# Kernel optimization log

Hardware: AMD Instinct MI355X
Metric: run time of the kernel (lower is better)

## Reference

```python
import jax, jax.numpy as jnp
import numpy as np

H = 16
E = 2048
LAT = E // 4
D = E // H          # 128
R = D // 2          # 64 (rotary dim)
B, S = 2, 2048

def _lin(x, W, b):
    return x @ W.T + b

def _rope_cos_sin(seq_len):
    inv_freq = 1.0 / (10000.0 ** (jnp.arange(0, R, 2, dtype=jnp.float32) / R))  # (R/2,)
    t = jnp.arange(seq_len, dtype=jnp.float32)
    freqs = jnp.outer(t, inv_freq)                 # (S, R/2)
    emb = jnp.concatenate([freqs, freqs], axis=-1) # (S, R)
    return jnp.cos(emb), jnp.sin(emb)

def _rotate_half(x):
    x1, x2 = x[..., : R // 2], x[..., R // 2 :]
    return jnp.concatenate([-x2, x1], axis=-1)

def _apply_rope(x, cos, sin):
    # x: (B, S, H, R); cos/sin: (S, R)
    c = cos[None, :, None, :]
    s = sin[None, :, None, :]
    return x * c + _rotate_half(x) * s

def setup_inputs() -> dict:
    key = jax.random.key(0)
    ks = jax.random.split(key, 20)
    def w(k, o, i):
        return jax.random.normal(k, (o, i), dtype=jnp.float32) * 0.02
    def bvec(k, o):
        return jax.random.normal(k, (o,), dtype=jnp.float32) * 0.02
    return {
        "x": jax.random.normal(ks[0], (B, S, E), dtype=jnp.float32),
        "Wkv_d": w(ks[1], LAT, E), "bkv_d": bvec(ks[2], LAT),
        "Wq_d": w(ks[3], LAT, E), "bq_d": bvec(ks[4], LAT),
        "Wk_u": w(ks[5], E // 2, LAT), "bk_u": bvec(ks[6], E // 2),
        "Wq_u": w(ks[7], E // 2, LAT), "bq_u": bvec(ks[8], E // 2),
        "Wv_u": w(ks[9], E, LAT), "bv_u": bvec(ks[10], E),
        "Wrk": w(ks[11], E // 2, E), "brk": bvec(ks[12], E // 2),
        "Wrq": w(ks[13], E // 2, LAT), "brq": bvec(ks[14], E // 2),
        "Wo": w(ks[15], E, E), "bo": bvec(ks[16], E),
    }

def reference(x, Wkv_d, bkv_d, Wq_d, bq_d, Wk_u, bk_u, Wq_u, bq_u,
              Wv_u, bv_u, Wrk, brk, Wrq, brq, Wo, bo):
    Bn, Sn, _ = x.shape
    kv_d = _lin(x, Wkv_d, bkv_d)                      # (B,S,LAT)
    q_d = _lin(x, Wq_d, bq_d)                         # (B,S,LAT)
    k1 = _lin(kv_d, Wk_u, bk_u).reshape(Bn, Sn, H, R)
    q1 = _lin(q_d, Wq_u, bq_u).reshape(Bn, Sn, H, R)
    v = _lin(kv_d, Wv_u, bv_u).reshape(Bn, Sn, H, D)
    kr = _lin(x, Wrk, brk).reshape(Bn, Sn, H, R)
    qr = _lin(q_d, Wrq, brq).reshape(Bn, Sn, H, R)
    cos, sin = _rope_cos_sin(Sn)
    qr = _apply_rope(qr, cos, sin)
    kr = _apply_rope(kr, cos, sin)
    k = jnp.concatenate([k1, kr], axis=-1)            # (B,S,H,D)
    q = jnp.concatenate([q1, qr], axis=-1)
    scale = 1.0 / np.sqrt(D)
    attn = jnp.einsum("bqhd,bkhd->bhqk", q, k) * scale
    attn = jax.nn.softmax(attn, axis=-1)
    out = jnp.einsum("bhqk,bkhd->bqhd", attn, v).reshape(Bn, Sn, E)
    return _lin(out, Wo, bo)
```

## Files before the change

kernel.cpp:

```cpp
#include <hip/hip_runtime.h>
#include <cmath>

typedef unsigned short ushort_t;
typedef unsigned int u32;
typedef __attribute__((ext_vector_type(8))) __bf16 bf16x8;
typedef __attribute__((ext_vector_type(4))) float f32x4;

#define Hh 16
#define Ss 2048
#define SCALE 0.08838834764831845f

__device__ __forceinline__ ushort_t f2bf(float f) {
  union { float f; unsigned u; } c; c.f = f;
  unsigned u = c.u;
  return (ushort_t)((u + 0x7FFFu + ((u >> 16) & 1u)) >> 16);
}
__device__ __forceinline__ float bf2f(ushort_t h) {
  union { unsigned u; float f; } c; c.u = ((unsigned)h) << 16;
  return c.f;
}
__device__ __forceinline__ u32 cvt_pk_bf16(float lo, float hi) {
  u32 r;
  asm volatile("v_cvt_pk_bf16_f32 %0, %1, %2" : "=v"(r) : "v"(lo), "v"(hi));
  return r;
}

__device__ __forceinline__ void gload_lds16(const ushort_t* g, ushort_t* l) {
  __builtin_amdgcn_global_load_lds(
      (const __attribute__((address_space(1))) u32*)g,
      (__attribute__((address_space(3))) u32*)l, 16, 0, 0);
}

struct SrcPtrs { const float* p[9]; };

__global__ __launch_bounds__(256) void convert_all_kernel(SrcPtrs sp,
    ushort_t* __restrict__ x_bf, ushort_t* __restrict__ wbuf) {
  const int cum[9] = {8192, 9216, 10240, 12288, 12800, 13824, 14336, 14848, 18944};
  const int dsto[9] = {0, 0, 1048576, 2097152, 4194304, 4718592, 5767168, 6291456, 6815744};
  const int bid = blockIdx.x;
  int s = 0;
  #pragma unroll
  for (int i = 0; i < 8; ++i) s += (bid >= cum[i]);
  const int lb = bid - (s == 0 ? 0 : cum[s - 1]);
  const float* src = sp.p[s] + (size_t)lb * 1024;
  ushort_t* dst = (s == 0 ? x_bf : wbuf + dsto[s]) + (size_t)lb * 1024;
  const int i = threadIdx.x * 4;
  float4 v = *(const float4*)&src[i];
  ushort4 o;
  o.x = f2bf(v.x); o.y = f2bf(v.y); o.z = f2bf(v.z); o.w = f2bf(v.w);
  *(ushort4*)&dst[i] = o;
}

template<int MODE, typename OUTT>
__global__ __launch_bounds__(256) void gemm_bf16(
    const ushort_t* __restrict__ A, const ushort_t* __restrict__ W,
    const float* __restrict__ bias, OUTT* __restrict__ C0,
    ushort_t* __restrict__ C1, int K)
{
  __shared__ ushort_t As[128][32];
  __shared__ ushort_t Bs[128][32];
  const int tid = threadIdx.x;
  const int lane = tid & 63;
  const int w = tid >> 6;
  const int wr = w >> 1, wc = w & 1;
  const int l15 = lane & 15, lhi = lane >> 4;
  const int m0 = blockIdx.y * 128, n0 = blockIdx.x * 128;

  const int srow = w * 16 + (lane >> 2);
  const int schunk = (lane & 3) * 8;

  f32x4 acc[4][4];
  #pragma unroll
  for (int i = 0; i < 4; ++i)
    #pragma unroll
    for (int j = 0; j < 4; ++j)
      acc[i][j] = (f32x4){0.f, 0.f, 0.f, 0.f};

  for (int k0 = 0; k0 < K; k0 += 32) {
    __syncthreads();
    gload_lds16(&A[(size_t)(m0 + srow) * K + k0 + schunk],       &As[w * 16][0]);
    gload_lds16(&A[(size_t)(m0 + 64 + srow) * K + k0 + schunk],  &As[64 + w * 16][0]);
    gload_lds16(&W[(size_t)(n0 + srow) * K + k0 + schunk],       &Bs[w * 16][0]);
    gload_lds16(&W[(size_t)(n0 + 64 + srow) * K + k0 + schunk],  &Bs[64 + w * 16][0]);
    __syncthreads();
    bf16x8 af[4], bfr[4];
    #pragma unroll
    for (int i = 0; i < 4; ++i) af[i] = *(const bf16x8*)&As[wr * 64 + i * 16 + l15][lhi * 8];
    #pragma unroll
    for (int j = 0; j < 4; ++j) bfr[j] = *(const bf16x8*)&Bs[wc * 64 + j * 16 + l15][lhi * 8];
    #pragma unroll
    for (int i = 0; i < 4; ++i)
      #pragma unroll
      for (int j = 0; j < 4; ++j)
        acc[i][j] = __builtin_amdgcn_mfma_f32_16x16x32_bf16(af[i], bfr[j], acc[i][j], 0, 0, 0);
  }

  #pragma unroll
  for (int i = 0; i < 4; ++i) {
    #pragma unroll
    for (int j = 0; j < 4; ++j) {
      const int n = n0 + wc * 64 + j * 16 + l15;
      const float bz = bias[n];
      #pragma unroll
      for (int r = 0; r < 4; ++r) {
        const int m = m0 + wr * 64 + i * 16 + lhi * 4 + r;
        const float v = acc[i][j][r] + bz;
        if constexpr (MODE == 0) {
          C0[(size_t)m * 2048 + n] = v;
        } else if constexpr (MODE == 2) {
          if (n < 1024)
            C0[(size_t)(n >> 9) * 2097152 + (size_t)m * 512 + (n & 511)] = (OUTT)f2bf(v);
          else {
            const int np = n - 1024;
            C1[(size_t)m * 2048 + (np >> 6) * 128 + (np & 63)] = f2bf(v);
          }
        } else if constexpr (MODE == 3) {
          if (n < 1024)
            C0[(size_t)m * 2048 + (n >> 6) * 128 + (n & 63)] = (OUTT)f2bf(v);
          else {
            const int np = n - 1024;
            C1[(size_t)(m >> 11) * 4194304 + (size_t)np * 2048 + (m & 2047)] = f2bf(v);
          }
        } else {
          const int np = n & 1023;
          C0[(size_t)m * 2048 + (np >> 6) * 128 + (np & 63) + ((n >> 10) << 6)] = (OUTT)f2bf(v);
        }
      }
    }
  }
}

__global__ __launch_bounds__(256) void rope_bf16_kernel(ushort_t* __restrict__ q,
                                                        ushort_t* __restrict__ k) {
  const int t = threadIdx.x & 63;
  const int idx = blockIdx.x * 4 + (threadIdx.x >> 6);
  const int s = (idx >> 4) & (Ss - 1);
  ushort_t* base = (t < 32 ? q : k) + (size_t)idx * 128 + 64;
  const int i = t & 31;
  const float invf = expf(-logf(10000.f) * (float)i / 32.f);
  const float fr = (float)s * invf;
  const float cs = cosf(fr), sn = sinf(fr);
  const float x1 = bf2f(base[i]);
  const float x2 = bf2f(base[i + 32]);
  base[i]      = f2bf(x1 * cs - x2 * sn);
  base[i + 32] = f2bf(x2 * cs + x1 * sn);
}

__global__ __launch_bounds__(256) void flash_mfma_kernel(
    const ushort_t* __restrict__ Qb, const ushort_t* __restrict__ Kb,
    const ushort_t* __restrict__ Vt, ushort_t* __restrict__ Oattn)
{
  __shared__ ushort_t Ks[64][136];
  __shared__ ushort_t Vs[128][72];
  __shared__ ushort_t Ps[4][32][72];

  const int tid = threadIdx.x, lane = tid & 63, w = tid >> 6;
  const int l15 = lane & 15, lhi = lane >> 4;
  const int bh = blockIdx.y, b = bh >> 4, h = bh & 15;
  const int q0 = blockIdx.x * 128 + w * 32;

  bf16x8 qf[2][4];
  #pragma unroll
  for (int mi = 0; mi < 2; ++mi) {
    const size_t qrow = (size_t)b * Ss + q0 + mi * 16 + l15;
    const ushort_t* qp = Qb + (qrow * Hh + h) * 128;
    #pragma unroll
    for (int dk = 0; dk < 4; ++dk)
      qf[mi][dk] = *(const bf16x8*)(qp + dk * 32 + lhi * 8);
  }

  f32x4 o[2][8];
  #pragma unroll
  for (int mi = 0; mi < 2; ++mi)
    #pragma unroll
    for (int dn = 0; dn < 8; ++dn) o[mi][dn] = (f32x4){0.f, 0.f, 0.f, 0.f};
  float lsum[2] = {0.f, 0.f};

  const size_t kbase_g = (size_t)b * Ss * 2048 + (size_t)h * 128;
  const size_t vbase_g = (size_t)bh * 128 * Ss;

  bf16x8 kv[4], vv[4];
  #pragma unroll
  for (int p = 0; p < 4; ++p) {
    const int idx = p * 256 + tid;
    kv[p] = *(const bf16x8*)&Kb[kbase_g + (size_t)(idx >> 4) * 2048 + (idx & 15) * 8];
    vv[p] = *(const bf16x8*)&Vt[vbase_g + (size_t)(idx >> 3) * Ss + (idx & 7) * 8];
  }

  for (int t = 0; t < Ss / 64; ++t) {
    __syncthreads();
    #pragma unroll
    for (int p = 0; p < 4; ++p) {
      const int idx = p * 256 + tid;
      *(bf16x8*)&Ks[idx >> 4][(idx & 15) * 8] = kv[p];
      *(bf16x8*)&Vs[idx >> 3][(idx & 7) * 8] = vv[p];
    }
    __syncthreads();

    if (t + 1 < Ss / 64) {
      const int s1 = (t + 1) * 64;
      #pragma unroll
      for (int p = 0; p < 4; ++p) {
        const int idx = p * 256 + tid;
        kv[p] = *(const bf16x8*)&Kb[kbase_g + (size_t)(s1 + (idx >> 4)) * 2048 + (idx & 15) * 8];
        vv[p] = *(const bf16x8*)&Vt[vbase_g + (size_t)(idx >> 3) * Ss + s1 + (idx & 7) * 8];
      }
    }

    f32x4 s[2][4];
    #pragma unroll
    for (int mi = 0; mi < 2; ++mi)
      #pragma unroll
      for (int jc = 0; jc < 4; ++jc) s[mi][jc] = (f32x4){0.f, 0.f, 0.f, 0.f};
    #pragma unroll
    for (int jc = 0; jc < 4; ++jc)
      #pragma unroll
      for (int dk = 0; dk < 4; ++dk) {
        bf16x8 ak = *(const bf16x8*)&Ks[jc * 16 + l15][dk * 32 + lhi * 8];
        s[0][jc] = __builtin_amdgcn_mfma_f32_16x16x32_bf16(ak, qf[0][dk], s[0][jc], 0, 0, 0);
        s[1][jc] = __builtin_amdgcn_mfma_f32_16x16x32_bf16(ak, qf[1][dk], s[1][jc], 0, 0, 0);
      }

    #pragma unroll
    for (int mi = 0; mi < 2; ++mi)
      #pragma unroll
      for (int jc = 0; jc < 4; ++jc) {
        const float p0 = __expf(s[mi][jc][0] * SCALE);
        const float p1 = __expf(s[mi][jc][1] * SCALE);
        const float p2 = __expf(s[mi][jc][2] * SCALE);
        const float p3 = __expf(s[mi][jc][3] * SCALE);
        lsum[mi] += (p0 + p1) + (p2 + p3);
        const u32 d0 = cvt_pk_bf16(p0, p1);
        const u32 d1 = cvt_pk_bf16(p2, p3);
        *(uint2*)&Ps[w][mi * 16 + l15][jc * 16 + lhi * 4] = make_uint2(d0, d1);
      }

    #pragma unroll
    for (int kc = 0; kc < 2; ++kc) {
      bf16x8 ap0 = *(const bf16x8*)&Ps[w][l15][kc * 32 + lhi * 8];
      bf16x8 ap1 = *(const bf16x8*)&Ps[w][16 + l15][kc * 32 + lhi * 8];
      #pragma unroll
      for (int dn = 0; dn < 8; ++dn) {
        bf16x8 bv = *(const bf16x8*)&Vs[dn * 16 + l15][kc * 32 + lhi * 8];
        o[0][dn] = __builtin_amdgcn_mfma_f32_16x16x32_bf16(ap0, bv, o[0][dn], 0, 0, 0);
        o[1][dn] = __builtin_amdgcn_mfma_f32_16x16x32_bf16(ap1, bv, o[1][dn], 0, 0, 0);
      }
    }
  }

  #pragma unroll
  for (int mi = 0; mi < 2; ++mi) {
    float v = lsum[mi];
    v += __shfl_xor(v, 16);
    v += __shfl_xor(v, 32);
    lsum[mi] = v;
  }

  #pragma unroll
  for (int mi = 0; mi < 2; ++mi) {
    float inv[4];
    #pragma unroll
    for (int r = 0; r < 4; ++r)
      inv[r] = 1.f / __shfl(lsum[mi], lhi * 4 + r);
    #pragma unroll
    for (int dn = 0; dn < 8; ++dn)
      #pragma unroll
      for (int r = 0; r < 4; ++r) {
        const int row = q0 + mi * 16 + lhi * 4 + r;
        const size_t addr = ((size_t)b * Ss + row) * 2048 + h * 128 + dn * 16 + l15;
        Oattn[addr] = f2bf(o[mi][dn][r] * inv[r]);
      }
  }
}

extern "C" void kernel_launch(void* const* d_in, const int* in_sizes, int n_in,
                              void* d_out, int out_size, void* d_ws, size_t ws_size,
                              hipStream_t stream)
{
  const float* x     = (const float*)d_in[0];
  const float* Wkv_d = (const float*)d_in[1];
  const float* bkv_d = (const float*)d_in[2];
  const float* Wq_d  = (const float*)d_in[3];
  const float* bq_d  = (const float*)d_in[4];
  const float* Wk_u  = (const float*)d_in[5];
  const float* bk_u  = (const float*)d_in[6];
  const float* Wq_u  = (const float*)d_in[7];
  const float* bq_u  = (const float*)d_in[8];
  const float* Wv_u  = (const float*)d_in[9];
  const float* bv_u  = (const float*)d_in[10];
  const float* Wrk   = (const float*)d_in[11];
  const float* brk   = (const float*)d_in[12];
  const float* Wrq   = (const float*)d_in[13];
  const float* brq   = (const float*)d_in[14];
  const float* Wo    = (const float*)d_in[15];
  const float* bo    = (const float*)d_in[16];

  ushort_t* ws = (ushort_t*)d_ws;
  ushort_t* x_bf  = ws;
  ushort_t* kv_d  = ws + 8388608;
  ushort_t* q_d   = ws + 10485760;
  ushort_t* qb    = ws + 12582912;
  ushort_t* kb    = ws + 20971520;
  ushort_t* vt    = ws + 29360128;
  ushort_t* attn  = ws + 37748736;
  ushort_t* wbuf  = ws + 46137344;
  float* bias_x  = (float*)(ws + 57147392);
  float* bias_kv = (float*)(ws + 57151488);
  float* bias_q  = (float*)(ws + 57157632);

  SrcPtrs sp;
  sp.p[0] = x;    sp.p[1] = Wkv_d; sp.p[2] = Wq_d; sp.p[3] = Wrk;
  sp.p[4] = Wk_u; sp.p[5] = Wv_u;  sp.p[6] = Wq_u; sp.p[7] = Wrq;
  sp.p[8] = Wo;
  convert_all_kernel<<<dim3(18944), dim3(256), 0, stream>>>(sp, x_bf, wbuf);

  hipMemcpyAsync(bias_x,         bkv_d, 512 * 4,  hipMemcpyDeviceToDevice, stream);
  hipMemcpyAsync(bias_x + 512,   bq_d,  512 * 4,  hipMemcpyDeviceToDevice, stream);
  hipMemcpyAsync(bias_x + 1024,  brk,   1024 * 4, hipMemcpyDeviceToDevice, stream);
  hipMemcpyAsync(bias_kv,        bk_u,  1024 * 4, hipMemcpyDeviceToDevice, stream);
  hipMemcpyAsync(bias_kv + 1024, bv_u,  2048 * 4, hipMemcpyDeviceToDevice, stream);
  hipMemcpyAsync(bias_q,         bq_u,  1024 * 4, hipMemcpyDeviceToDevice, stream);
  hipMemcpyAsync(bias_q + 1024,  brq,   1024 * 4, hipMemcpyDeviceToDevice, stream);

  const dim3 blk(256);

  gemm_bf16<2, ushort_t><<<dim3(16, 32), blk, 0, stream>>>(
      x_bf, wbuf, bias_x, kv_d, kb + 64, 2048);
  gemm_bf16<3, ushort_t><<<dim3(24, 32), blk, 0, stream>>>(
      kv_d, wbuf + 4194304, bias_kv, kb, vt, 512);
  gemm_bf16<4, ushort_t><<<dim3(16, 32), blk, 0, stream>>>(
      q_d, wbuf + 5767168, bias_q, qb, nullptr, 512);

  rope_bf16_kernel<<<dim3(Ss * Hh * 2 / 4), blk, 0, stream>>>(qb, kb);

  flash_mfma_kernel<<<dim3(Ss / 128, 32), blk, 0, stream>>>(qb, kb, vt, attn);

  gemm_bf16<0, float><<<dim3(16, 32), blk, 0, stream>>>(
      attn, wbuf + 6815744, bo, (float*)d_out, nullptr, 2048);
}
```

Measured before the change: 292.1 us.

## Double-buffer flash K/V tiles, keep P in registers, merge up-projection GEMMs

The flash attention kernel now double-buffers its K/V tiles in LDS, which needs one barrier per iteration instead of two. It rebuilds the probability MFMA operand in registers with permlane swaps instead of bouncing it through a per-wave LDS buffer. The K/V and Q up-projection GEMMs are merged into one launch that switches its A pointer by column block. This removes a kernel launch and some LDS traffic, at the cost of more LDS per block and correctness that depends on the permlane layout and the block-dependent A offset.

```diff
diff --git a/kernel.cpp b/kernel.cpp
--- a/kernel.cpp
+++ b/kernel.cpp
@@ -55,7 +55,7 @@
 __global__ __launch_bounds__(256) void gemm_bf16(
     const ushort_t* __restrict__ A, const ushort_t* __restrict__ W,
     const float* __restrict__ bias, OUTT* __restrict__ C0,
-    ushort_t* __restrict__ C1, int K)
+    ushort_t* __restrict__ C1, ushort_t* __restrict__ C2, int K)
 {
   __shared__ ushort_t As[128][32];
   __shared__ ushort_t Bs[128][32];
@@ -65,6 +65,8 @@
   const int wr = w >> 1, wc = w & 1;
   const int l15 = lane & 15, lhi = lane >> 4;
   const int m0 = blockIdx.y * 128, n0 = blockIdx.x * 128;
+
+  if constexpr (MODE == 5) { if (blockIdx.x >= 24) A += 2097152; }
 
   const int srow = w * 16 + (lane >> 2);
   const int schunk = (lane & 3) * 8;
@@ -114,16 +116,17 @@
             const int np = n - 1024;
             C1[(size_t)m * 2048 + (np >> 6) * 128 + (np & 63)] = f2bf(v);
           }
-        } else if constexpr (MODE == 3) {
-          if (n < 1024)
+        } else {
+          if (n < 1024) {
             C0[(size_t)m * 2048 + (n >> 6) * 128 + (n & 63)] = (OUTT)f2bf(v);
-          else {
+          } else if (n < 3072) {
             const int np = n - 1024;
             C1[(size_t)(m >> 11) * 4194304 + (size_t)np * 2048 + (m & 2047)] = f2bf(v);
+          } else {
+            const int np = n - 3072;
+            const int col = ((np & 1023) >> 6) * 128 + (np & 63) + ((np >> 10) << 6);
+            C2[(size_t)m * 2048 + col] = f2bf(v);
           }
-        } else {
-          const int np = n & 1023;
-          C0[(size_t)m * 2048 + (np >> 6) * 128 + (np & 63) + ((n >> 10) << 6)] = (OUTT)f2bf(v);
         }
       }
     }
@@ -150,9 +153,8 @@
     const ushort_t* __restrict__ Qb, const ushort_t* __restrict__ Kb,
     const ushort_t* __restrict__ Vt, ushort_t* __restrict__ Oattn)
 {
-  __shared__ ushort_t Ks[64][136];
-  __shared__ ushort_t Vs[128][72];
-  __shared__ ushort_t Ps[4][32][72];
+  __shared__ ushort_t Ks[2][64][136];
+  __shared__ ushort_t Vs[2][128][72];
 
   const int tid = threadIdx.x, lane = tid & 63, w = tid >> 6;
   const int l15 = lane & 15, lhi = lane >> 4;
@@ -180,32 +182,32 @@
   const size_t vbase_g = (size_t)bh * 128 * Ss;
 
   bf16x8 kv[4], vv[4];
-  #pragma unroll
-  for (int p = 0; p < 4; ++p) {
-    const int idx = p * 256 + tid;
-    kv[p] = *(const bf16x8*)&Kb[kbase_g + (size_t)(idx >> 4) * 2048 + (idx & 15) * 8];
-    vv[p] = *(const bf16x8*)&Vt[vbase_g + (size_t)(idx >> 3) * Ss + (idx & 7) * 8];
-  }
-
-  for (int t = 0; t < Ss / 64; ++t) {
-    __syncthreads();
+  auto load_tile = [&](int s0) {
     #pragma unroll
     for (int p = 0; p < 4; ++p) {
       const int idx = p * 256 + tid;
-      *(bf16x8*)&Ks[idx >> 4][(idx & 15) * 8] = kv[p];
-      *(bf16x8*)&Vs[idx >> 3][(idx & 7) * 8] = vv[p];
+      kv[p] = *(const bf16x8*)&Kb[kbase_g + (size_t)(s0 + (idx >> 4)) * 2048 + (idx & 15) * 8];
+      vv[p] = *(const bf16x8*)&Vt[vbase_g + (size_t)(idx >> 3) * Ss + s0 + (idx & 7) * 8];
     }
-    __syncthreads();
-
-    if (t + 1 < Ss / 64) {
-      const int s1 = (t + 1) * 64;
-      #pragma unroll
-      for (int p = 0; p < 4; ++p) {
-        const int idx = p * 256 + tid;
-        kv[p] = *(const bf16x8*)&Kb[kbase_g + (size_t)(s1 + (idx >> 4)) * 2048 + (idx & 15) * 8];
-        vv[p] = *(const bf16x8*)&Vt[vbase_g + (size_t)(idx >> 3) * Ss + s1 + (idx & 7) * 8];
-      }
+  };
+  auto write_tile = [&](int buf) {
+    #pragma unroll
+    for (int p = 0; p < 4; ++p) {
+      const int idx = p * 256 + tid;
+      *(bf16x8*)&Ks[buf][idx >> 4][(idx & 15) * 8] = kv[p];
+      *(bf16x8*)&Vs[buf][idx >> 3][(idx & 7) * 8] = vv[p];
     }
+  };
+
+  load_tile(0);
+  write_tile(0);
+  load_tile(64);
+  __syncthreads();
+
+  for (int t = 0; t < Ss / 64; ++t) {
+    const int cur = t & 1, nxt = cur ^ 1;
+    write_tile(nxt);
+    load_tile(t + 2 < Ss / 64 ? (t + 2) * 64 : Ss - 64);
 
     f32x4 s[2][4];
     #pragma unroll
@@ -216,13 +218,14 @@
     for (int jc = 0; jc < 4; ++jc)
       #pragma unroll
       for (int dk = 0; dk < 4; ++dk) {
-        bf16x8 ak = *(const bf16x8*)&Ks[jc * 16 + l15][dk * 32 + lhi * 8];
+        bf16x8 ak = *(const bf16x8*)&Ks[cur][jc * 16 + l15][dk * 32 + lhi * 8];
         s[0][jc] = __builtin_amdgcn_mfma_f32_16x16x32_bf16(ak, qf[0][dk], s[0][jc], 0, 0, 0);
         s[1][jc] = __builtin_amdgcn_mfma_f32_16x16x32_bf16(ak, qf[1][dk], s[1][jc], 0, 0, 0);
       }
 
     #pragma unroll
-    for (int mi = 0; mi < 2; ++mi)
+    for (int mi = 0; mi < 2; ++mi) {
+      u32 D0[4], D1[4];
       #pragma unroll
       for (int jc = 0; jc < 4; ++jc) {
         const float p0 = __expf(s[mi][jc][0] * SCALE);
@@ -230,22 +233,27 @@
         const float p2 = __expf(s[mi][jc][2] * SCALE);
         const float p3 = __expf(s[mi][jc][3] * SCALE);
         lsum[mi] += (p0 + p1) + (p2 + p3);
-        const u32 d0 = cvt_pk_bf16(p0, p1);
-        const u32 d1 = cvt_pk_bf16(p2, p3);
-        *(uint2*)&Ps[w][mi * 16 + l15][jc * 16 + lhi * 4] = make_uint2(d0, d1);
-      }
-
-    #pragma unroll
-    for (int kc = 0; kc < 2; ++kc) {
-      bf16x8 ap0 = *(const bf16x8*)&Ps[w][l15][kc * 32 + lhi * 8];
-      bf16x8 ap1 = *(const bf16x8*)&Ps[w][16 + l15][kc * 32 + lhi * 8];
-      #pragma unroll
-      for (int dn = 0; dn < 8; ++dn) {
-        bf16x8 bv = *(const bf16x8*)&Vs[dn * 16 + l15][kc * 32 + lhi * 8];
-        o[0][dn] = __builtin_amdgcn_mfma_f32_16x16x32_bf16(ap0, bv, o[0][dn], 0, 0, 0);
-        o[1][dn] = __builtin_amdgcn_mfma_f32_16x16x32_bf16(ap1, bv, o[1][dn], 0, 0, 0);
+        D0[jc] = cvt_pk_bf16(p0, p1);
+        D1[jc] = cvt_pk_bf16(p2, p3);
+      }
+      #pragma unroll
+      for (int kc = 0; kc < 2; ++kc) {
+        u32 X = D0[2 * kc], Xp = D0[2 * kc + 1];
+        u32 Y = D1[2 * kc], Yp = D1[2 * kc + 1];
+        asm volatile("v_permlane32_swap_b32 %0, %1" : "+v"(X), "+v"(Xp));
+        asm volatile("v_permlane16_swap_b32 %0, %1" : "+v"(X), "+v"(Xp));
+        asm volatile("v_permlane32_swap_b32 %0, %1" : "+v"(Y), "+v"(Yp));
+        asm volatile("v_permlane16_swap_b32 %0, %1" : "+v"(Y), "+v"(Yp));
+        union { u32 u[4]; bf16x8 v; } ap;
+        ap.u[0] = X; ap.u[1] = Y; ap.u[2] = Xp; ap.u[3] = Yp;
+        #pragma unroll
+        for (int dn = 0; dn < 8; ++dn) {
+          bf16x8 bv = *(const bf16x8*)&Vs[cur][dn * 16 + l15][kc * 32 + lhi * 8];
+          o[mi][dn] = __builtin_amdgcn_mfma_f32_16x16x32_bf16(ap.v, bv, o[mi][dn], 0, 0, 0);
+        }
       }
     }
+    __syncthreads();
   }
 
   #pragma unroll
@@ -304,9 +312,8 @@
   ushort_t* vt    = ws + 29360128;
   ushort_t* attn  = ws + 37748736;
   ushort_t* wbuf  = ws + 46137344;
-  float* bias_x  = (float*)(ws + 57147392);
-  float* bias_kv = (float*)(ws + 57151488);
-  float* bias_q  = (float*)(ws + 57157632);
+  float* bias_x   = (float*)(ws + 57147392);
+  float* bias_kvq = (float*)(ws + 57151488);
 
   SrcPtrs sp;
   sp.p[0] = x;    sp.p[1] = Wkv_d; sp.p[2] = Wq_d; sp.p[3] = Wrk;
@@ -314,27 +321,25 @@
   sp.p[8] = Wo;
   convert_all_kernel<<<dim3(18944), dim3(256), 0, stream>>>(sp, x_bf, wbuf);
 
-  hipMemcpyAsync(bias_x,         bkv_d, 512 * 4,  hipMemcpyDeviceToDevice, stream);
-  hipMemcpyAsync(bias_x + 512,   bq_d,  512 * 4,  hipMemcpyDeviceToDevice, stream);
-  hipMemcpyAsync(bias_x + 1024,  brk,   1024 * 4, hipMemcpyDeviceToDevice, stream);
-  hipMemcpyAsync(bias_kv,        bk_u,  1024 * 4, hipMemcpyDeviceToDevice, stream);
-  hipMemcpyAsync(bias_kv + 1024, bv_u,  2048 * 4, hipMemcpyDeviceToDevice, stream);
-  hipMemcpyAsync(bias_q,         bq_u,  1024 * 4, hipMemcpyDeviceToDevice, stream);
-  hipMemcpyAsync(bias_q + 1024,  brq,   1024 * 4, hipMemcpyDeviceToDevice, stream);
+  hipMemcpyAsync(bias_x,          bkv_d, 512 * 4,  hipMemcpyDeviceToDevice, stream);
+  hipMemcpyAsync(bias_x + 512,    bq_d,  512 * 4,  hipMemcpyDeviceToDevice, stream);
+  hipMemcpyAsync(bias_x + 1024,   brk,   1024 * 4, hipMemcpyDeviceToDevice, stream);
+  hipMemcpyAsync(bias_kvq,        bk_u,  1024 * 4, hipMemcpyDeviceToDevice, stream);
+  hipMemcpyAsync(bias_kvq + 1024, bv_u,  2048 * 4, hipMemcpyDeviceToDevice, stream);
+  hipMemcpyAsync(bias_kvq + 3072, bq_u,  1024 * 4, hipMemcpyDeviceToDevice, stream);
+  hipMemcpyAsync(bias_kvq + 4096, brq,   1024 * 4, hipMemcpyDeviceToDevice, stream);
 
   const dim3 blk(256);
 
   gemm_bf16<2, ushort_t><<<dim3(16, 32), blk, 0, stream>>>(
-      x_bf, wbuf, bias_x, kv_d, kb + 64, 2048);
-  gemm_bf16<3, ushort_t><<<dim3(24, 32), blk, 0, stream>>>(
-      kv_d, wbuf + 4194304, bias_kv, kb, vt, 512);
-  gemm_bf16<4, ushort_t><<<dim3(16, 32), blk, 0, stream>>>(
-      q_d, wbuf + 5767168, bias_q, qb, nullptr, 512);
+      x_bf, wbuf, bias_x, kv_d, kb + 64, nullptr, 2048);
+  gemm_bf16<5, ushort_t><<<dim3(40, 32), blk, 0, stream>>>(
+      kv_d, wbuf + 4194304, bias_kvq, kb, vt, qb, 512);
 
   rope_bf16_kernel<<<dim3(Ss * Hh * 2 / 4), blk, 0, stream>>>(qb, kb);
 
   flash_mfma_kernel<<<dim3(Ss / 128, 32), blk, 0, stream>>>(qb, kb, vt, attn);
 
   gemm_bf16<0, float><<<dim3(16, 32), blk, 0, stream>>>(
-      attn, wbuf + 6815744, bo, (float*)d_out, nullptr, 2048);
-}
+      attn, wbuf + 6815744, bo, (float*)d_out, nullptr, nullptr, 2048);
+}
```

Measured after the change: 327.9 us. 1.12x slower.

## Merge kv/q up-projection GEMMs into one launch and deepen K tile to 64

Applied to the files above, without the earlier changes.

Combines the two up-projection GEMMs (kv_d→k/v and q_d→q) into a single launch with 40 column blocks. Blocks past column 24 offset the A pointer to q_d and write into qb through a new third output pointer. The GEMM K-step also doubles from 32 to 64 with wider LDS tiles, which halves the number of barrier pairs per tile. The aim is less launch overhead, a better-filled grid and lower sync cost, at the price of twice the LDS per block, which could reduce occupancy.

```diff
diff --git a/kernel.cpp b/kernel.cpp
--- a/kernel.cpp
+++ b/kernel.cpp
@@ -55,10 +55,10 @@
 __global__ __launch_bounds__(256) void gemm_bf16(
     const ushort_t* __restrict__ A, const ushort_t* __restrict__ W,
     const float* __restrict__ bias, OUTT* __restrict__ C0,
-    ushort_t* __restrict__ C1, int K)
+    ushort_t* __restrict__ C1, ushort_t* __restrict__ C2, int K)
 {
-  __shared__ ushort_t As[128][32];
-  __shared__ ushort_t Bs[128][32];
+  __shared__ ushort_t As[128][64];
+  __shared__ ushort_t Bs[128][64];
   const int tid = threadIdx.x;
   const int lane = tid & 63;
   const int w = tid >> 6;
@@ -66,8 +66,10 @@
   const int l15 = lane & 15, lhi = lane >> 4;
   const int m0 = blockIdx.y * 128, n0 = blockIdx.x * 128;
 
-  const int srow = w * 16 + (lane >> 2);
-  const int schunk = (lane & 3) * 8;
+  if constexpr (MODE == 5) { if (blockIdx.x >= 24) A += 2097152; }
+
+  const int srow_base = w * 8 + (lane >> 3);
+  const int scol = (lane & 7) * 8;
 
   f32x4 acc[4][4];
   #pragma unroll
@@ -76,23 +78,30 @@
     for (int j = 0; j < 4; ++j)
       acc[i][j] = (f32x4){0.f, 0.f, 0.f, 0.f};
 
-  for (int k0 = 0; k0 < K; k0 += 32) {
+  for (int k0 = 0; k0 < K; k0 += 64) {
     __syncthreads();
-    gload_lds16(&A[(size_t)(m0 + srow) * K + k0 + schunk],       &As[w * 16][0]);
-    gload_lds16(&A[(size_t)(m0 + 64 + srow) * K + k0 + schunk],  &As[64 + w * 16][0]);
-    gload_lds16(&W[(size_t)(n0 + srow) * K + k0 + schunk],       &Bs[w * 16][0]);
-    gload_lds16(&W[(size_t)(n0 + 64 + srow) * K + k0 + schunk],  &Bs[64 + w * 16][0]);
+    #pragma unroll
+    for (int q = 0; q < 4; ++q) {
+      const int row = q * 32 + srow_base;
+      gload_lds16(&A[(size_t)(m0 + row) * K + k0 + scol], &As[q * 32 + w * 8][0]);
+      gload_lds16(&W[(size_t)(n0 + row) * K + k0 + scol], &Bs[q * 32 + w * 8][0]);
+    }
     __syncthreads();
-    bf16x8 af[4], bfr[4];
-    #pragma unroll
-    for (int i = 0; i < 4; ++i) af[i] = *(const bf16x8*)&As[wr * 64 + i * 16 + l15][lhi * 8];
-    #pragma unroll
-    for (int j = 0; j < 4; ++j) bfr[j] = *(const bf16x8*)&Bs[wc * 64 + j * 16 + l15][lhi * 8];
-    #pragma unroll
-    for (int i = 0; i < 4; ++i)
+    #pragma unroll
+    for (int dk = 0; dk < 2; ++dk) {
+      bf16x8 af[4], bfr[4];
+      #pragma unroll
+      for (int i = 0; i < 4; ++i)
+        af[i] = *(const bf16x8*)&As[wr * 64 + i * 16 + l15][dk * 32 + lhi * 8];
       #pragma unroll
       for (int j = 0; j < 4; ++j)
-        acc[i][j] = __builtin_amdgcn_mfma_f32_16x16x32_bf16(af[i], bfr[j], acc[i][j], 0, 0, 0);
+        bfr[j] = *(const bf16x8*)&Bs[wc * 64 + j * 16 + l15][dk * 32 + lhi * 8];
+      #pragma unroll
+      for (int i = 0; i < 4; ++i)
+        #pragma unroll
+        for (int j = 0; j < 4; ++j)
+          acc[i][j] = __builtin_amdgcn_mfma_f32_16x16x32_bf16(af[i], bfr[j], acc[i][j], 0, 0, 0);
+    }
   }
 
   #pragma unroll
@@ -114,16 +123,17 @@
             const int np = n - 1024;
             C1[(size_t)m * 2048 + (np >> 6) * 128 + (np & 63)] = f2bf(v);
           }
-        } else if constexpr (MODE == 3) {
-          if (n < 1024)
+        } else {
+          if (n < 1024) {
             C0[(size_t)m * 2048 + (n >> 6) * 128 + (n & 63)] = (OUTT)f2bf(v);
-          else {
+          } else if (n < 3072) {
             const int np = n - 1024;
             C1[(size_t)(m >> 11) * 4194304 + (size_t)np * 2048 + (m & 2047)] = f2bf(v);
+          } else {
+            const int np = n - 3072;
+            const int col = ((np & 1023) >> 6) * 128 + (np & 63) + ((np >> 10) << 6);
+            C2[(size_t)m * 2048 + col] = f2bf(v);
           }
-        } else {
-          const int np = n & 1023;
-          C0[(size_t)m * 2048 + (np >> 6) * 128 + (np & 63) + ((n >> 10) << 6)] = (OUTT)f2bf(v);
         }
       }
     }
@@ -304,9 +314,8 @@
   ushort_t* vt    = ws + 29360128;
   ushort_t* attn  = ws + 37748736;
   ushort_t* wbuf  = ws + 46137344;
-  float* bias_x  = (float*)(ws + 57147392);
-  float* bias_kv = (float*)(ws + 57151488);
-  float* bias_q  = (float*)(ws + 57157632);
+  float* bias_x   = (float*)(ws + 57147392);
+  float* bias_kvq = (float*)(ws + 57151488);
 
   SrcPtrs sp;
   sp.p[0] = x;    sp.p[1] = Wkv_d; sp.p[2] = Wq_d; sp.p[3] = Wrk;
@@ -314,27 +323,25 @@
   sp.p[8] = Wo;
   convert_all_kernel<<<dim3(18944), dim3(256), 0, stream>>>(sp, x_bf, wbuf);
 
-  hipMemcpyAsync(bias_x,         bkv_d, 512 * 4,  hipMemcpyDeviceToDevice, stream);
-  hipMemcpyAsync(bias_x + 512,   bq_d,  512 * 4,  hipMemcpyDeviceToDevice, stream);
-  hipMemcpyAsync(bias_x + 1024,  brk,   1024 * 4, hipMemcpyDeviceToDevice, stream);
-  hipMemcpyAsync(bias_kv,        bk_u,  1024 * 4, hipMemcpyDeviceToDevice, stream);
-  hipMemcpyAsync(bias_kv + 1024, bv_u,  2048 * 4, hipMemcpyDeviceToDevice, stream);
-  hipMemcpyAsync(bias_q,         bq_u,  1024 * 4, hipMemcpyDeviceToDevice, stream);
-  hipMemcpyAsync(bias_q + 1024,  brq,   1024 * 4, hipMemcpyDeviceToDevice, stream);
+  hipMemcpyAsync(bias_x,          bkv_d, 512 * 4,  hipMemcpyDeviceToDevice, stream);
+  hipMemcpyAsync(bias_x + 512,    bq_d,  512 * 4,  hipMemcpyDeviceToDevice, stream);
+  hipMemcpyAsync(bias_x + 1024,   brk,   1024 * 4, hipMemcpyDeviceToDevice, stream);
+  hipMemcpyAsync(bias_kvq,        bk_u,  1024 * 4, hipMemcpyDeviceToDevice, stream);
+  hipMemcpyAsync(bias_kvq + 1024, bv_u,  2048 * 4, hipMemcpyDeviceToDevice, stream);
+  hipMemcpyAsync(bias_kvq + 3072, bq_u,  1024 * 4, hipMemcpyDeviceToDevice, stream);
+  hipMemcpyAsync(bias_kvq + 4096, brq,   1024 * 4, hipMemcpyDeviceToDevice, stream);
 
   const dim3 blk(256);
 
   gemm_bf16<2, ushort_t><<<dim3(16, 32), blk, 0, stream>>>(
-      x_bf, wbuf, bias_x, kv_d, kb + 64, 2048);
-  gemm_bf16<3, ushort_t><<<dim3(24, 32), blk, 0, stream>>>(
-      kv_d, wbuf + 4194304, bias_kv, kb, vt, 512);
-  gemm_bf16<4, ushort_t><<<dim3(16, 32), blk, 0, stream>>>(
-      q_d, wbuf + 5767168, bias_q, qb, nullptr, 512);
+      x_bf, wbuf, bias_x, kv_d, kb + 64, nullptr, 2048);
+  gemm_bf16<5, ushort_t><<<dim3(40, 32), blk, 0, stream>>>(
+      kv_d, wbuf + 4194304, bias_kvq, kb, vt, qb, 512);
 
   rope_bf16_kernel<<<dim3(Ss * Hh * 2 / 4), blk, 0, stream>>>(qb, kb);
 
   flash_mfma_kernel<<<dim3(Ss / 128, 32), blk, 0, stream>>>(qb, kb, vt, attn);
 
   gemm_bf16<0, float><<<dim3(16, 32), blk, 0, stream>>>(
-      attn, wbuf + 6815744, bo, (float*)d_out, nullptr, 2048);
-}
+      attn, wbuf + 6815744, bo, (float*)d_out, nullptr, nullptr, 2048);
+}
```

Result: no change. 292.0 us (-0.0%).
